# Kernel optimization log

Hardware: AMD Instinct MI355X
Metric: run time of the kernel (lower is better)

Reference implementation:

```python
import jax, jax.numpy as jnp
import numpy as np

VOCAB = 100000
EMB = 256
HID = 512
NTAGS = 16
START = 14
STOP = 15
SEQ = 4096
NEG = -10000.0


def setup_inputs() -> dict:
    key = jax.random.key(0)
    ks = jax.random.split(key, 16)
    s = 1.0 / np.sqrt(HID)
    u = lambda k, shape: jax.random.uniform(k, shape, jnp.float32, -s, s)
    sentence = jax.random.randint(ks[0], (SEQ,), 0, VOCAB)
    emb = jax.random.normal(ks[1], (VOCAB, EMB), jnp.float32) * 0.02
    # per-direction GRU params, torch layout: W_ih [3H,E], W_hh [3H,H]
    Wih_f = u(ks[2], (3 * HID, EMB)); Whh_f = u(ks[3], (3 * HID, HID))
    bih_f = u(ks[4], (3 * HID,));     bhh_f = u(ks[5], (3 * HID,))
    Wih_b = u(ks[6], (3 * HID, EMB)); Whh_b = u(ks[7], (3 * HID, HID))
    bih_b = u(ks[8], (3 * HID,));     bhh_b = u(ks[9], (3 * HID,))
    Wout = u(ks[10], (NTAGS, HID)); bout = u(ks[11], (NTAGS,))
    transition = jax.random.normal(ks[12], (NTAGS, NTAGS), jnp.float32)
    transition = transition.at[START, :].set(NEG)  # nothing transitions TO start... (to-start row)
    transition = transition.at[:, STOP].set(NEG)   # nothing transitions FROM stop
    return {"sentence": sentence, "emb": emb,
            "Wih_f": Wih_f, "Whh_f": Whh_f, "bih_f": bih_f, "bhh_f": bhh_f,
            "Wih_b": Wih_b, "Whh_b": Whh_b, "bih_b": bih_b, "bhh_b": bhh_b,
            "Wout": Wout, "bout": bout, "transition": transition}


def _gru_dir(x, Wih, Whh, bih, bhh):
    # x: [S, E] -> hidden states [S, H]; torch GRU cell math
    xp = x @ Wih.T + bih  # [S, 3H], precomputed input projections

    def step(h, xt):
        hp = h @ Whh.T + bhh
        xr, xz, xn = jnp.split(xt, 3)
        hr, hz, hn = jnp.split(hp, 3)
        r = jax.nn.sigmoid(xr + hr)
        z = jax.nn.sigmoid(xz + hz)
        n = jnp.tanh(xn + r * hn)
        h_new = (1.0 - z) * n + z * h
        return h_new, h_new

    h0 = jnp.zeros((HID,), x.dtype)
    _, hs = jax.lax.scan(step, h0, xp)
    return hs


def _features(sentence, emb, Wih_f, Whh_f, bih_f, bhh_f, Wih_b, Whh_b, bih_b, bhh_b, Wout, bout):
    x = emb[sentence]  # [S, E]
    h_fwd = _gru_dir(x, Wih_f, Whh_f, bih_f, bhh_f)
    h_bwd = _gru_dir(x[::-1], Wih_b, Whh_b, bih_b, bhh_b)[::-1]
    h = h_fwd + h_bwd  # module sums the two direction halves
    return h @ Wout.T + bout  # [S, NTAGS]


def _viterbi(feats, transition):
    init = jnp.full((NTAGS,), -1000.0, feats.dtype).at[START].set(0.0)

    def step(fv, feat):
        scores = fv[None, :] + transition  # [next, prev]
        bp = jnp.argmax(scores, axis=1)    # best prev per next tag
        vit = jnp.max(scores, axis=1)
        return vit + feat, bp

    fv, bps = jax.lax.scan(step, init, feats)  # bps: [S, NTAGS]
    terminal = fv + transition[STOP]
    best = jnp.argmax(terminal)
    score = terminal[best]

    def back(tag, bp):
        prev = bp[tag]
        return prev, prev

    _, prevs = jax.lax.scan(back, best, bps, reverse=True)  # prevs[i] = tag at time i-1
    path = jnp.concatenate([prevs[1:], best[None]])  # drop START, append final tag
    return score, path


def reference(sentence, emb, Wih_f, Whh_f, bih_f, bhh_f, Wih_b, Whh_b, bih_b, bhh_b, Wout, bout, transition):
    feats = _features(sentence, emb, Wih_f, Whh_f, bih_f, bhh_f,
                      Wih_b, Whh_b, bih_b, bhh_b, Wout, bout)
    score, path = _viterbi(feats, transition)
    return score, path
```

## Files before the change

### kernel.cpp

```cpp
#include <hip/hip_runtime.h>
#include <stdint.h>

#define SEQ   4096
#define EMB   256
#define HID   512
#define NTAGS 16
#define START_TAG 14
#define STOP_TAG  15
#define MAGICW 0x9E3779B1u

__global__ __launch_bounds__(256) void k_xp(
    const int* __restrict__ sent, const float* __restrict__ emb,
    const float* __restrict__ WihF, const float* __restrict__ bihF,
    const float* __restrict__ WihB, const float* __restrict__ bihB,
    float* __restrict__ xp)
{
  __shared__ float XsT[64 * 72];
  __shared__ float WsT[64 * 132];

  const int tid = threadIdx.x;
  const int dir = blockIdx.z;
  const float* Wih = dir ? WihB : WihF;
  const float* bih = dir ? bihB : bihF;

  const int tl = tid & 63, q = tid >> 6;
  const int tg = blockIdx.x * 64 + tl;
  const int srow = dir ? (SEQ - 1 - tg) : tg;
  const float* xrow = emb + (size_t)sent[srow] * EMB;

  const int r = tid >> 1, hh = tid & 1;
  const float* wrow = Wih + (size_t)(blockIdx.y * 128 + r) * EMB;

  const int cx = tid & 31, ty = tid >> 5;
  float acc[8][4] = {};

  for (int kc = 0; kc < 4; kc++) {
    const int kb = kc * 64;
    __syncthreads();
    #pragma unroll
    for (int i = 0; i < 4; i++) {
      float4 v = *(const float4*)(xrow + kb + q * 16 + i * 4);
      int kk = q * 16 + i * 4;
      XsT[(kk + 0) * 72 + tl] = v.x; XsT[(kk + 1) * 72 + tl] = v.y;
      XsT[(kk + 2) * 72 + tl] = v.z; XsT[(kk + 3) * 72 + tl] = v.w;
    }
    #pragma unroll
    for (int i = 0; i < 8; i++) {
      float4 v = *(const float4*)(wrow + kb + hh * 32 + i * 4);
      int kk = hh * 32 + i * 4;
      WsT[(kk + 0) * 132 + r] = v.x; WsT[(kk + 1) * 132 + r] = v.y;
      WsT[(kk + 2) * 132 + r] = v.z; WsT[(kk + 3) * 132 + r] = v.w;
    }
    __syncthreads();
    #pragma unroll 4
    for (int kk = 0; kk < 64; kk++) {
      const float4 b  = *(const float4*)&WsT[kk * 132 + cx * 4];
      const float4 x0 = *(const float4*)&XsT[kk * 72 + ty * 8];
      const float4 x1 = *(const float4*)&XsT[kk * 72 + ty * 8 + 4];
      const float av[8] = {x0.x, x0.y, x0.z, x0.w, x1.x, x1.y, x1.z, x1.w};
      const float bv[4] = {b.x, b.y, b.z, b.w};
      #pragma unroll
      for (int i = 0; i < 8; i++)
        #pragma unroll
        for (int j = 0; j < 4; j++)
          acc[i][j] = fmaf(av[i], bv[j], acc[i][j]);
    }
  }

  const float4 bv4 = *(const float4*)(bih + blockIdx.y * 128 + cx * 4);
  #pragma unroll
  for (int i = 0; i < 8; i++) {
    int t = blockIdx.x * 64 + ty * 8 + i;
    float4 o;
    o.x = acc[i][0] + bv4.x; o.y = acc[i][1] + bv4.y;
    o.z = acc[i][2] + bv4.z; o.w = acc[i][3] + bv4.w;
    *(float4*)(xp + ((size_t)dir * SEQ + t) * 1536 + blockIdx.y * 128 + cx * 4) = o;
  }
}

__device__ __forceinline__ int pidx(int k) { return (k >> 6) * 68 + (k & 63); }

__global__ __launch_bounds__(256, 1) void k_rec(
    const float* __restrict__ WhhF, const float* __restrict__ bhhF,
    const float* __restrict__ WhhB, const float* __restrict__ bhhB,
    const float* __restrict__ xp,
    unsigned long long* __restrict__ hcomm)
{
  const int wg  = blockIdx.x;
  const int dir = wg >> 5;
  const int g   = wg & 31;
  const int Cbase = g * 16;
  const int tid = threadIdx.x;
  const int rg = tid >> 4, kq = tid & 15;

  const float* Whh = dir ? WhhB : WhhF;
  const float* bhh = dir ? bhhB : bhhF;
  const float* xpd = xp + (size_t)dir * SEQ * 1536;
  unsigned long long* hcd = hcomm + (size_t)dir * SEQ * HID;

  __shared__ float h_shf[8 * 68];
  __shared__ float dsg[48];

  float4 w4[3][8];
  #pragma unroll
  for (int j = 0; j < 3; j++) {
    int rl = rg * 3 + j;
    int gate = rl >> 4, il = rl & 15;
    const float* wr = Whh + (size_t)(gate * HID + Cbase + il) * HID + kq * 32;
    #pragma unroll
    for (int qq = 0; qq < 8; qq++) w4[j][qq] = *(const float4*)(wr + qq * 4);
  }
  float b3x = 0.f, b3y = 0.f, b3z = 0.f;
  if (tid < 16) {
    b3x = bhh[Cbase + tid];
    b3y = bhh[HID + Cbase + tid];
    b3z = bhh[2 * HID + Cbase + tid];
  }

  const int w0 = tid, w1 = tid + 256;
  const bool own0 = (w0 >= Cbase && w0 < Cbase + 16);
  const bool own1 = (w1 >= Cbase && w1 < Cbase + 16);

  h_shf[pidx(w0)] = 0.f;
  h_shf[pidx(w1)] = 0.f;
  __syncthreads();

  for (int t = 0; t < SEQ; t++) {
    float xr = 0.f, xz = 0.f, xn = 0.f;
    if (tid < 16) {
      const float* xt = xpd + (size_t)t * 1536;
      xr = xt[Cbase + tid];
      xz = xt[HID + Cbase + tid];
      xn = xt[2 * HID + Cbase + tid];
    }

    if (t > 0) {
      unsigned long long* src = hcd + (size_t)(t - 1) * HID;
      bool n0 = !own0, n1 = !own1;
      while (n0 | n1) {
        if (n0) {
          unsigned long long v = __hip_atomic_load(src + w0, __ATOMIC_RELAXED, __HIP_MEMORY_SCOPE_AGENT);
          if ((unsigned)(v >> 32) == MAGICW) {
            h_shf[pidx(w0)] = __uint_as_float((unsigned)(v & 0xffffffffull)); n0 = false;
          }
        }
        if (n1) {
          unsigned long long v = __hip_atomic_load(src + w1, __ATOMIC_RELAXED, __HIP_MEMORY_SCOPE_AGENT);
          if ((unsigned)(v >> 32) == MAGICW) {
            h_shf[pidx(w1)] = __uint_as_float((unsigned)(v & 0xffffffffull)); n1 = false;
          }
        }
      }
    }
    __syncthreads();

    float hprev = 0.f;
    if (tid < 16) hprev = h_shf[pidx(Cbase + tid)];

    float a0 = 0.f, a1 = 0.f, a2 = 0.f;
    {
      const float4* hs4 = (const float4*)h_shf;
      const int b4 = (kq >> 1) * 17 + (kq & 1) * 8;
      #pragma unroll
      for (int qq = 0; qq < 8; qq++) {
        float4 hv = hs4[b4 + qq];
        a0 = fmaf(w4[0][qq].x, hv.x, a0); a0 = fmaf(w4[0][qq].y, hv.y, a0);
        a0 = fmaf(w4[0][qq].z, hv.z, a0); a0 = fmaf(w4[0][qq].w, hv.w, a0);
        a1 = fmaf(w4[1][qq].x, hv.x, a1); a1 = fmaf(w4[1][qq].y, hv.y, a1);
        a1 = fmaf(w4[1][qq].z, hv.z, a1); a1 = fmaf(w4[1][qq].w, hv.w, a1);
        a2 = fmaf(w4[2][qq].x, hv.x, a2); a2 = fmaf(w4[2][qq].y, hv.y, a2);
        a2 = fmaf(w4[2][qq].z, hv.z, a2); a2 = fmaf(w4[2][qq].w, hv.w, a2);
      }
    }
    #pragma unroll
    for (int m = 1; m < 16; m <<= 1) {
      a0 += __shfl_xor(a0, m); a1 += __shfl_xor(a1, m); a2 += __shfl_xor(a2, m);
    }
    if (kq == 0) {
      dsg[rg * 3 + 0] = a0; dsg[rg * 3 + 1] = a1; dsg[rg * 3 + 2] = a2;
    }
    __syncthreads();

    if (tid < 16) {
      float hr = dsg[tid], hz = dsg[16 + tid], hn = dsg[32 + tid];
      float rr = 1.f / (1.f + expf(-(xr + hr + b3x)));
      float zz = 1.f / (1.f + expf(-(xz + hz + b3y)));
      float nn = tanhf(xn + rr * (hn + b3z));
      float hnew = (1.f - zz) * nn + zz * hprev;
      h_shf[pidx(Cbase + tid)] = hnew;
      unsigned long long pv = ((unsigned long long)MAGICW << 32) |
                              (unsigned long long)__float_as_uint(hnew);
      __hip_atomic_store(&hcd[(size_t)t * HID + Cbase + tid], pv,
                         __ATOMIC_RELAXED, __HIP_MEMORY_SCOPE_AGENT);
    }
  }
}

__global__ __launch_bounds__(256) void k_feats(
    const unsigned long long* __restrict__ hcomm,
    const float* __restrict__ Wout, const float* __restrict__ bout,
    float* __restrict__ feats)
{
  __shared__ float hs[16 * 516];
  const int tid = threadIdx.x, bt = blockIdx.x;

  {
    const unsigned long long* hf = hcomm;
    const unsigned long long* hb = hcomm + (size_t)SEQ * HID;
    #pragma unroll 8
    for (int i = 0; i < 32; i++) {
      int e = i * 256 + tid;
      int tl = e >> 9, k = e & 511;
      int t = bt * 16 + tl;
      float vf = __uint_as_float((unsigned)(hf[(size_t)t * HID + k] & 0xffffffffull));
      float vb = __uint_as_float((unsigned)(hb[(size_t)(SEQ - 1 - t) * HID + k] & 0xffffffffull));
      hs[tl * 516 + k] = vf + vb;
    }
  }
  __syncthreads();

  const int tag = tid & 15, tl = tid >> 4;
  const float4* h4  = (const float4*)&hs[tl * 516];
  const float4* w4p = (const float4*)(Wout + (size_t)tag * HID);
  float acc = 0.f;
  #pragma unroll 8
  for (int qq = 0; qq < 128; qq++) {
    float4 a = h4[qq], b = w4p[qq];
    acc = fmaf(a.x, b.x, acc); acc = fmaf(a.y, b.y, acc);
    acc = fmaf(a.z, b.z, acc); acc = fmaf(a.w, b.w, acc);
  }
  int t = bt * 16 + tl;
  feats[t * NTAGS + tag] = acc + bout[tag];
}

__device__ __forceinline__ unsigned long long compose_map(
    unsigned long long A, unsigned long long B)
{
  unsigned long long r = 0ull;
  #pragma unroll
  for (int i = 0; i < 16; i++) {
    int bi = (int)((B >> (4 * i)) & 15ull);
    unsigned long long ai = (A >> (4 * bi)) & 15ull;
    r |= ai << (4 * i);
  }
  return r;
}

__device__ __forceinline__ unsigned long long pack16(uint4 w)
{
  auto pk = [](unsigned v) -> unsigned {
    unsigned x = v & 0x0F0F0F0Fu;
    unsigned t = x | (x >> 4);
    return (t & 0xFFu) | ((t >> 8) & 0xFF00u);
  };
  return (unsigned long long)pk(w.x) | ((unsigned long long)pk(w.y) << 16) |
         ((unsigned long long)pk(w.z) << 32) | ((unsigned long long)pk(w.w) << 48);
}

__global__ __launch_bounds__(64, 1) void k_vit(
    const float* __restrict__ feats, const float* __restrict__ trans,
    unsigned char* __restrict__ bps, float* __restrict__ out)
{
  const int lane = threadIdx.x;
  const int nx = lane >> 2, pg = lane & 3;

  const float tr0 = trans[nx * 16 + pg * 4 + 0];
  const float tr1 = trans[nx * 16 + pg * 4 + 1];
  const float tr2 = trans[nx * 16 + pg * 4 + 2];
  const float tr3 = trans[nx * 16 + pg * 4 + 3];

  float f0 = (pg * 4 + 0) == START_TAG ? 0.f : -1000.f;
  float f1 = (pg * 4 + 1) == START_TAG ? 0.f : -1000.f;
  float f2 = (pg * 4 + 2) == START_TAG ? 0.f : -1000.f;
  float f3 = (pg * 4 + 3) == START_TAG ? 0.f : -1000.f;

  float ft = feats[nx];
  for (int t = 0; t < SEQ; t++) {
    float ftn = feats[(t + 1 < SEQ ? t + 1 : t) * NTAGS + nx];
    float best = f0 + tr0; int bi = pg * 4;
    float c1 = f1 + tr1; if (c1 > best) { best = c1; bi = pg * 4 + 1; }
    float c2 = f2 + tr2; if (c2 > best) { best = c2; bi = pg * 4 + 2; }
    float c3 = f3 + tr3; if (c3 > best) { best = c3; bi = pg * 4 + 3; }
    #pragma unroll
    for (int m = 1; m <= 2; m <<= 1) {
      float ov = __shfl_xor(best, m);
      int   oi = __shfl_xor(bi, m);
      if (ov > best || (ov == best && oi < bi)) { best = ov; bi = oi; }
    }
    float fvnew = best + ft;
    if (pg == 0) bps[t * 16 + nx] = (unsigned char)bi;
    f0 = __shfl(fvnew, (pg * 4 + 0) << 2);
    f1 = __shfl(fvnew, (pg * 4 + 1) << 2);
    f2 = __shfl(fvnew, (pg * 4 + 2) << 2);
    f3 = __shfl(fvnew, (pg * 4 + 3) << 2);
    ft = ftn;
  }

  float g0 = __shfl(f0, nx);
  float g1 = __shfl(f1, nx);
  float g2 = __shfl(f2, nx);
  float g3 = __shfl(f3, nx);
  int b2 = lane & 3;
  float fvl = (b2 == 0) ? g0 : (b2 == 1) ? g1 : (b2 == 2) ? g2 : g3;
  float term = (lane < 16) ? (fvl + trans[STOP_TAG * 16 + lane]) : -3.0e38f;
  int ti = (lane < 16) ? lane : 99;
  #pragma unroll
  for (int m = 1; m <= 32; m <<= 1) {
    float ov = __shfl_xor(term, m);
    int   oi = __shfl_xor(ti, m);
    if (ov > term || (ov == term && oi < ti)) { term = ov; ti = oi; }
  }
  if (lane == 0) out[0] = term;
  const int best = ti;

  __threadfence_block();

  const uint4* bp4 = (const uint4*)bps;
  const unsigned long long IDENT = 0xFEDCBA9876543210ull;
  unsigned long long R = IDENT;
  {
    uint4 w = bp4[lane * 64 + 63];
    for (int s = 63; s >= 0; s--) {
      uint4 wn = (s > 0) ? bp4[lane * 64 + s - 1] : w;
      R = compose_map(pack16(w), R);
      w = wn;
    }
  }
  unsigned long long I = R;
  #pragma unroll
  for (int d = 1; d < 64; d <<= 1) {
    unsigned long long o = __shfl_down(I, d);
    if (lane + d < 64) I = compose_map(I, o);
  }
  unsigned long long E = __shfl_down(I, 1);
  if (lane == 63) E = IDENT;

  int cur = (int)((E >> (4 * best)) & 15ull);
  {
    uint4 w = bp4[lane * 64 + 63];
    for (int s = 63; s >= 0; s--) {
      int t = lane * 64 + s;
      uint4 wn = (s > 0) ? bp4[t - 1] : w;
      out[1 + t] = (float)cur;
      unsigned word = (cur < 4) ? w.x : (cur < 8) ? w.y : (cur < 12) ? w.z : w.w;
      cur = (int)((word >> ((cur & 3) * 8)) & 15u);
      w = wn;
    }
  }
}

extern "C" void kernel_launch(void* const* d_in, const int* in_sizes, int n_in,
                              void* d_out, int out_size, void* d_ws, size_t ws_size,
                              hipStream_t stream)
{
  const int*   sent  = (const int*)d_in[0];
  const float* emb   = (const float*)d_in[1];
  const float* WihF  = (const float*)d_in[2];
  const float* WhhF  = (const float*)d_in[3];
  const float* bihF  = (const float*)d_in[4];
  const float* bhhF  = (const float*)d_in[5];
  const float* WihB  = (const float*)d_in[6];
  const float* WhhB  = (const float*)d_in[7];
  const float* bihB  = (const float*)d_in[8];
  const float* bhhB  = (const float*)d_in[9];
  const float* Wout  = (const float*)d_in[10];
  const float* bout  = (const float*)d_in[11];
  const float* trans = (const float*)d_in[12];
  float* out = (float*)d_out;

  char* ws = (char*)d_ws;
  const size_t xp_bytes = (size_t)2 * SEQ * 1536 * 4;
  const size_t hc_bytes = (size_t)2 * SEQ * HID * 8;
  const size_t ft_bytes = (size_t)SEQ * NTAGS * 4;
  float*              xp    = (float*)ws;
  unsigned long long* hcomm = (unsigned long long*)(ws + xp_bytes);
  float*              feats = (float*)(ws + xp_bytes + hc_bytes);
  unsigned char*      bps   = (unsigned char*)(ws + xp_bytes + hc_bytes + ft_bytes);

  hipMemsetAsync(hcomm, 0, hc_bytes, stream);

  k_xp  <<<dim3(64, 12, 2), 256, 0, stream>>>(sent, emb, WihF, bihF, WihB, bihB, xp);
  k_rec <<<64, 256, 0, stream>>>(WhhF, bhhF, WhhB, bhhB, xp, hcomm);
  k_feats<<<256, 256, 0, stream>>>(hcomm, Wout, bout, feats);
  k_vit <<<1, 64, 0, stream>>>(feats, trans, bps, out);
}
```

Baseline: 8.786 ms.

## Remove shared-memory staging and barriers from GRU recurrence step

Each thread now polls the 32 flagged hidden values it needs straight from global memory into registers, so the shared h buffer and both per-step __syncthreads go away. The work split changes so each 16-lane group owns one hidden unit across all three gates. The lane with kq==0 then finishes the gate math with no trip through shared memory. The trade is that every thread issues 32 atomic 64-bit loads per step, sixteen times the previous global traffic, which may add polling contention and register pressure on the sequential critical path.

```diff
diff --git a/kernel.cpp b/kernel.cpp
--- a/kernel.cpp
+++ b/kernel.cpp
@@ -78,8 +78,6 @@
   }
 }
 
-__device__ __forceinline__ int pidx(int k) { return (k >> 6) * 68 + (k & 63); }
-
 __global__ __launch_bounds__(256, 1) void k_rec(
     const float* __restrict__ WhhF, const float* __restrict__ bhhF,
     const float* __restrict__ WhhB, const float* __restrict__ bhhB,
@@ -91,106 +89,89 @@
   const int g   = wg & 31;
   const int Cbase = g * 16;
   const int tid = threadIdx.x;
-  const int rg = tid >> 4, kq = tid & 15;
+  const int idx = tid >> 4;
+  const int kq  = tid & 15;
 
   const float* Whh = dir ? WhhB : WhhF;
   const float* bhh = dir ? bhhB : bhhF;
   const float* xpd = xp + (size_t)dir * SEQ * 1536;
   unsigned long long* hcd = hcomm + (size_t)dir * SEQ * HID;
 
-  __shared__ float h_shf[8 * 68];
-  __shared__ float dsg[48];
+  const int hi = Cbase + idx;
 
   float4 w4[3][8];
   #pragma unroll
   for (int j = 0; j < 3; j++) {
-    int rl = rg * 3 + j;
-    int gate = rl >> 4, il = rl & 15;
-    const float* wr = Whh + (size_t)(gate * HID + Cbase + il) * HID + kq * 32;
+    const float* wr = Whh + (size_t)(j * HID + hi) * HID + kq * 32;
     #pragma unroll
     for (int qq = 0; qq < 8; qq++) w4[j][qq] = *(const float4*)(wr + qq * 4);
   }
+  const bool epi = (kq == 0);
   float b3x = 0.f, b3y = 0.f, b3z = 0.f;
-  if (tid < 16) {
-    b3x = bhh[Cbase + tid];
-    b3y = bhh[HID + Cbase + tid];
-    b3z = bhh[2 * HID + Cbase + tid];
-  }
-
-  const int w0 = tid, w1 = tid + 256;
-  const bool own0 = (w0 >= Cbase && w0 < Cbase + 16);
-  const bool own1 = (w1 >= Cbase && w1 < Cbase + 16);
-
-  h_shf[pidx(w0)] = 0.f;
-  h_shf[pidx(w1)] = 0.f;
-  __syncthreads();
+  if (epi) {
+    b3x = bhh[hi];
+    b3y = bhh[HID + hi];
+    b3z = bhh[2 * HID + hi];
+  }
+
+  float hprev = 0.f;
 
   for (int t = 0; t < SEQ; t++) {
     float xr = 0.f, xz = 0.f, xn = 0.f;
-    if (tid < 16) {
+    if (epi) {
       const float* xt = xpd + (size_t)t * 1536;
-      xr = xt[Cbase + tid];
-      xz = xt[HID + Cbase + tid];
-      xn = xt[2 * HID + Cbase + tid];
-    }
-
+      xr = xt[hi];
+      xz = xt[HID + hi];
+      xn = xt[2 * HID + hi];
+    }
+
+    float a0 = 0.f, a1 = 0.f, a2 = 0.f;
     if (t > 0) {
-      unsigned long long* src = hcd + (size_t)(t - 1) * HID;
-      bool n0 = !own0, n1 = !own1;
-      while (n0 | n1) {
-        if (n0) {
-          unsigned long long v = __hip_atomic_load(src + w0, __ATOMIC_RELAXED, __HIP_MEMORY_SCOPE_AGENT);
-          if ((unsigned)(v >> 32) == MAGICW) {
-            h_shf[pidx(w0)] = __uint_as_float((unsigned)(v & 0xffffffffull)); n0 = false;
-          }
-        }
-        if (n1) {
-          unsigned long long v = __hip_atomic_load(src + w1, __ATOMIC_RELAXED, __HIP_MEMORY_SCOPE_AGENT);
-          if ((unsigned)(v >> 32) == MAGICW) {
-            h_shf[pidx(w1)] = __uint_as_float((unsigned)(v & 0xffffffffull)); n1 = false;
-          }
-        }
+      const unsigned long long* src = hcd + (size_t)(t - 1) * HID + kq * 32;
+      unsigned long long v[32];
+      #pragma unroll
+      for (int s = 0; s < 32; s++)
+        v[s] = __hip_atomic_load(src + s, __ATOMIC_RELAXED, __HIP_MEMORY_SCOPE_AGENT);
+      for (;;) {
+        unsigned miss = 0u;
+        #pragma unroll
+        for (int s = 0; s < 32; s++)
+          if ((unsigned)(v[s] >> 32) != MAGICW) miss |= (1u << s);
+        if (!miss) break;
+        #pragma unroll
+        for (int s = 0; s < 32; s++)
+          if (miss & (1u << s))
+            v[s] = __hip_atomic_load(src + s, __ATOMIC_RELAXED, __HIP_MEMORY_SCOPE_AGENT);
       }
-    }
-    __syncthreads();
-
-    float hprev = 0.f;
-    if (tid < 16) hprev = h_shf[pidx(Cbase + tid)];
-
-    float a0 = 0.f, a1 = 0.f, a2 = 0.f;
-    {
-      const float4* hs4 = (const float4*)h_shf;
-      const int b4 = (kq >> 1) * 17 + (kq & 1) * 8;
       #pragma unroll
       for (int qq = 0; qq < 8; qq++) {
-        float4 hv = hs4[b4 + qq];
-        a0 = fmaf(w4[0][qq].x, hv.x, a0); a0 = fmaf(w4[0][qq].y, hv.y, a0);
-        a0 = fmaf(w4[0][qq].z, hv.z, a0); a0 = fmaf(w4[0][qq].w, hv.w, a0);
-        a1 = fmaf(w4[1][qq].x, hv.x, a1); a1 = fmaf(w4[1][qq].y, hv.y, a1);
-        a1 = fmaf(w4[1][qq].z, hv.z, a1); a1 = fmaf(w4[1][qq].w, hv.w, a1);
-        a2 = fmaf(w4[2][qq].x, hv.x, a2); a2 = fmaf(w4[2][qq].y, hv.y, a2);
-        a2 = fmaf(w4[2][qq].z, hv.z, a2); a2 = fmaf(w4[2][qq].w, hv.w, a2);
+        float hv[4];
+        #pragma unroll
+        for (int c = 0; c < 4; c++)
+          hv[c] = __uint_as_float((unsigned)(v[qq * 4 + c] & 0xffffffffull));
+        a0 = fmaf(w4[0][qq].x, hv[0], a0); a0 = fmaf(w4[0][qq].y, hv[1], a0);
+        a0 = fmaf(w4[0][qq].z, hv[2], a0); a0 = fmaf(w4[0][qq].w, hv[3], a0);
+        a1 = fmaf(w4[1][qq].x, hv[0], a1); a1 = fmaf(w4[1][qq].y, hv[1], a1);
+        a1 = fmaf(w4[1][qq].z, hv[2], a1); a1 = fmaf(w4[1][qq].w, hv[3], a1);
+        a2 = fmaf(w4[2][qq].x, hv[0], a2); a2 = fmaf(w4[2][qq].y, hv[1], a2);
+        a2 = fmaf(w4[2][qq].z, hv[2], a2); a2 = fmaf(w4[2][qq].w, hv[3], a2);
       }
     }
+
     #pragma unroll
     for (int m = 1; m < 16; m <<= 1) {
       a0 += __shfl_xor(a0, m); a1 += __shfl_xor(a1, m); a2 += __shfl_xor(a2, m);
     }
-    if (kq == 0) {
-      dsg[rg * 3 + 0] = a0; dsg[rg * 3 + 1] = a1; dsg[rg * 3 + 2] = a2;
-    }
-    __syncthreads();
-
-    if (tid < 16) {
-      float hr = dsg[tid], hz = dsg[16 + tid], hn = dsg[32 + tid];
-      float rr = 1.f / (1.f + expf(-(xr + hr + b3x)));
-      float zz = 1.f / (1.f + expf(-(xz + hz + b3y)));
-      float nn = tanhf(xn + rr * (hn + b3z));
+
+    if (epi) {
+      float rr = 1.f / (1.f + expf(-(xr + a0 + b3x)));
+      float zz = 1.f / (1.f + expf(-(xz + a1 + b3y)));
+      float nn = tanhf(xn + rr * (a2 + b3z));
       float hnew = (1.f - zz) * nn + zz * hprev;
-      h_shf[pidx(Cbase + tid)] = hnew;
+      hprev = hnew;
       unsigned long long pv = ((unsigned long long)MAGICW << 32) |
                               (unsigned long long)__float_as_uint(hnew);
-      __hip_atomic_store(&hcd[(size_t)t * HID + Cbase + tid], pv,
+      __hip_atomic_store(&hcd[(size_t)t * HID + hi], pv,
                          __ATOMIC_RELAXED, __HIP_MEMORY_SCOPE_AGENT);
     }
   }
```

Measured after the change: 32.12 ms. +265.6%, slower.
